# Optimization experiments

Measured on AMD Instinct MI355X. Metric: run time of the kernel, lower is better.

The kernel has to match this reference:

```python
import jax, jax.numpy as jnp
import numpy as np
from jax import lax

B, T, V, E, H = 8, 512, 32000, 256, 512
NEG = -1e9


def setup_inputs() -> dict:
    key = jax.random.key(0)
    ks = jax.random.split(key, 13)
    g = lambda k, shp, sc: (jax.random.normal(k, shp, jnp.float32) * sc)
    return {
        'x': jax.random.randint(ks[0], (B, T), 0, V),
        'lengths': jax.random.randint(ks[1], (B,), T // 2, T + 1),
        'embed': g(ks[2], (V, E), 0.02),
        'W_ih': g(ks[3], (H, E), 1.0 / np.sqrt(E)),
        'W_hh': g(ks[4], (H, H), 1.0 / np.sqrt(H)),
        'b_ih': g(ks[5], (H,), 0.01),
        'b_hh': g(ks[6], (H,), 0.01),
        'attn_W': g(ks[7], (H, 2 * H), 1.0 / np.sqrt(2 * H)),
        'attn_b': g(ks[8], (H,), 0.01),
        'attn_v': g(ks[9], (1, H), 1.0 / np.sqrt(H)),
        'attn_v_b': g(ks[10], (1,), 0.01),
        'fc_W': g(ks[11], (V, 2 * H), 1.0 / np.sqrt(2 * H)),
        'fc_b': g(ks[12], (V,), 0.01),
    }


def reference(x, lengths, embed, W_ih, W_hh, b_ih, b_hh,
              attn_W, attn_b, attn_v, attn_v_b, fc_W, fc_b):
    b, t = x.shape
    h = W_ih.shape[0]
    # embedding with padding_idx=0 (row 0 forced to zero)
    tab = embed.at[0].set(0.0)
    emb = tab[x]  # [B,T,E]
    # vanilla tanh RNN via scan (precompute input projection)
    xin = emb @ W_ih.T + b_ih  # [B,T,H]

    def rnn_step(hprev, xt):
        hnew = jnp.tanh(xt + hprev @ W_hh.T + b_hh)
        return hnew, hnew

    _, out = lax.scan(rnn_step, jnp.zeros((b, h), xin.dtype), xin.transpose(1, 0, 2))
    out = out.transpose(1, 0, 2)  # [B,T,H]
    # pad_packed_sequence zeros hidden states past each sequence length
    len_mask = jnp.arange(t)[None, :] < lengths[:, None]  # [B,T]
    out = out * len_mask[..., None].astype(out.dtype)

    # additive attention: score(t,s) = v . tanh(W1 h_t + W2 h_s + b)
    W1, W2 = attn_W[:, :h], attn_W[:, h:]
    q = out @ W1.T            # [B,T,H]
    k = out @ W2.T + attn_b   # [B,T,H]
    v = attn_v[0]             # [H]

    def att_row(_, qt):  # qt: [B,H] -> scores over all s: [B,T]
        s = jnp.tanh(qt[:, None, :] + k) @ v + attn_v_b[0]
        return None, s

    _, scores = lax.scan(att_row, None, q.transpose(1, 0, 2))  # [T,B,T]
    scores = scores.transpose(1, 0, 2)  # [B,T(query),T(key)]
    causal = jnp.arange(t)[:, None] >= jnp.arange(t)[None, :]  # s <= t
    valid = causal[None] & len_mask[:, None, :]
    scores = jnp.where(valid, scores, NEG)
    alpha = jax.nn.softmax(scores, axis=-1)
    context = jnp.einsum('bts,bsh->bth', alpha, out)  # [B,T,H]
    feats = jnp.concatenate([out, context], axis=-1)  # [B,T,2H]
    logits = feats @ fc_W.T + fc_b  # [B,T,V]
    return logits
```

## Files before the change

kernel.cpp:

```cpp
#include <hip/hip_runtime.h>
#include <hip/hip_bf16.h>

typedef __attribute__((ext_vector_type(8))) short short8;
typedef __attribute__((ext_vector_type(4))) float f32x4;
typedef __attribute__((ext_vector_type(4))) unsigned int u32x4;

__device__ __forceinline__ void glds16(const void* g, void* l) {
  __builtin_amdgcn_global_load_lds(
      (const __attribute__((address_space(1))) unsigned int*)g,
      (__attribute__((address_space(3))) unsigned int*)l, 16, 0, 0);
}

__device__ __forceinline__ void bar_lds() {
  asm volatile("s_waitcnt lgkmcnt(0)\n\ts_barrier" ::: "memory");
}

__device__ __forceinline__ float fast_tanh(float x) {
  float e = __expf(2.0f * x);
  return (e - 1.0f) * __builtin_amdgcn_rcpf(e + 1.0f);
}

__device__ __forceinline__ unsigned short bfh(float f) {
  __hip_bfloat16 h = __float2bfloat16(f);
  return *reinterpret_cast<unsigned short*>(&h);
}
__device__ __forceinline__ float bf2f(unsigned short u) {
  unsigned v = ((unsigned)u) << 16;
  float f;
  __builtin_memcpy(&f, &v, 4);
  return f;
}
__device__ __forceinline__ short bf16r(float f) { return (short)bfh(f); }

union FragU {
  unsigned int u[4];
  short8 s;
};

__global__ __launch_bounds__(256) void k_xin(const int* __restrict__ x, const float* __restrict__ embed,
                                             const float* __restrict__ W_ih, const float* __restrict__ b_ih,
                                             float* __restrict__ xin) {
  __shared__ float At[64][128];
  __shared__ float Bt[128][64];
  const int tid = threadIdx.x;
  const int bt0 = blockIdx.x * 64, j0 = blockIdx.y * 64;
  const int ty = tid >> 4, tx = tid & 15;
  const int lane = tid & 63, cgrp = tid >> 6;
  float acc[4][4] = {};
  for (int kc = 0; kc < 256; kc += 128) {
#pragma unroll
    for (int rr = 0; rr < 8; ++rr) {
      int row = rr * 8 + (tid >> 5);
      int col = (tid & 31) * 4;
      int tok = x[bt0 + row];
      float4 v = make_float4(0.f, 0.f, 0.f, 0.f);
      if (tok != 0) v = *(const float4*)&embed[(size_t)tok * 256 + kc + col];
      *(float4*)&At[row][col] = v;
    }
#pragma unroll
    for (int cc = 0; cc < 8; ++cc) {
      int col = cgrp * 32 + cc * 4;
      float4 v = *(const float4*)&W_ih[(size_t)(j0 + lane) * 256 + kc + col];
      Bt[col + 0][lane] = v.x; Bt[col + 1][lane] = v.y;
      Bt[col + 2][lane] = v.z; Bt[col + 3][lane] = v.w;
    }
    __syncthreads();
    for (int kk = 0; kk < 128; ++kk) {
      float bv[4];
#pragma unroll
      for (int c = 0; c < 4; ++c) bv[c] = Bt[kk][tx * 4 + c];
#pragma unroll
      for (int a = 0; a < 4; ++a) {
        float av = At[ty * 4 + a][kk];
#pragma unroll
        for (int c = 0; c < 4; ++c) acc[a][c] = fmaf(av, bv[c], acc[a][c]);
      }
    }
    __syncthreads();
  }
#pragma unroll
  for (int a = 0; a < 4; ++a) {
    int m = bt0 + ty * 4 + a;
#pragma unroll
    for (int c = 0; c < 4; ++c) {
      int j = j0 + tx * 4 + c;
      xin[(size_t)m * 512 + j] = acc[a][c] + b_ih[j];
    }
  }
}

__global__ __launch_bounds__(512) void k_rnn(const float* __restrict__ xin, const float* __restrict__ W_hh,
                                             const float* __restrict__ b_hh, const int* __restrict__ lengths,
                                             unsigned long long* mbox, float* __restrict__ out,
                                             unsigned short* __restrict__ feats,
                                             const float* __restrict__ fcW, unsigned short* __restrict__ fcWb) {
  const int tid = threadIdx.x;
  if (blockIdx.x >= 8) {
    const size_t stride = (size_t)(gridDim.x - 8) * 512 * 8;
    for (size_t i = ((size_t)(blockIdx.x - 8) * 512 + tid) * 8; i < 32768000ull; i += stride) {
      float4 a = *(const float4*)(fcW + i);
      float4 b = *(const float4*)(fcW + i + 4);
      short8 v;
      v[0] = bf16r(a.x); v[1] = bf16r(a.y); v[2] = bf16r(a.z); v[3] = bf16r(a.w);
      v[4] = bf16r(b.x); v[5] = bf16r(b.y); v[6] = bf16r(b.z); v[7] = bf16r(b.w);
      *(short8*)(fcWb + i) = v;
    }
    return;
  }
  const int blk = blockIdx.x;
  const int w = tid >> 6, l = tid & 63;
  const int jt = w & 3, kh = w >> 2;
  const int j16 = blk * 64 + jt * 16;
  const int r = l & 15;
  const int g = l >> 4;
  const int n = l & 15;

  __shared__ unsigned long long stg[2048];
  __shared__ f32x4 Cbuf[4][64];
  __shared__ float hLf[8][64];
  __shared__ unsigned int hL32[8][64];
  __shared__ int nflag[2];

  short8 bhi[8], blo[8];
  {
    const float* wrow = &W_hh[(size_t)(j16 + n) * 512];
#pragma unroll
    for (int c8 = 0; c8 < 8; ++c8) {
      int c = kh * 8 + c8;
      const float* wp = wrow + c * 32 + g * 8;
      float4 wa = *(const float4*)wp;
      float4 wb = *(const float4*)(wp + 4);
      float wv[8] = {wa.x, wa.y, wa.z, wa.w, wb.x, wb.y, wb.z, wb.w};
#pragma unroll
      for (int e = 0; e < 8; ++e) {
        unsigned short h = bfh(wv[e]);
        bhi[c8][e] = (short)h;
        blo[c8][e] = (short)bfh(wv[e] - bf2f(h));
      }
    }
  }

  float bj = 0.f, xv[4];
  if (w < 4 && l < 32) {
    bj = b_hh[j16 + n];
#pragma unroll
    for (int i = 0; i < 4; ++i)
      xv[i] = xin[((size_t)(g * 4 + i) * 512 + 0) * 512 + j16 + n];
  }
  const int mylen = lengths[(tid >> 6) & 7];

  if (tid < 2) nflag[tid] = 0;
  __syncthreads();

  const int sgran = tid ^ ((tid >> 6) & 3);

  for (int t = 0; t < 512; ++t) {
    {
      unsigned long long* src = mbox + ((size_t)blk * 16 + (t & 15)) * 2048 + tid * 4;
      bool mine = false;
      int round = 0;
      while (true) {
        if (!mine) {
          u32x4 A, B2;
          asm volatile(
              "global_load_dwordx4 %0, %2, off sc0 sc1\n\t"
              "global_load_dwordx4 %1, %2, off offset:16 sc0 sc1\n\t"
              "s_waitcnt vmcnt(0)"
              : "=&v"(A), "=&v"(B2)
              : "v"(src)
              : "memory");
          bool ok = true;
#pragma unroll
          for (int q = 0; q < 4; ++q) ok = ok && (A[q] != 0xFFFFFFFFu) && (B2[q] != 0xFFFFFFFFu);
          if (ok) {
            mine = true;
            stg[sgran * 4 + 0] = (unsigned long long)A[0] | ((unsigned long long)A[1] << 32);
            stg[sgran * 4 + 1] = (unsigned long long)A[2] | ((unsigned long long)A[3] << 32);
            stg[sgran * 4 + 2] = (unsigned long long)B2[0] | ((unsigned long long)B2[1] << 32);
            stg[sgran * 4 + 3] = (unsigned long long)B2[2] | ((unsigned long long)B2[3] << 32);
            u32x4 S;
            S[0] = S[1] = S[2] = S[3] = 0xFFFFFFFFu;
            asm volatile(
                "global_store_dwordx4 %0, %1, off sc0 sc1\n\t"
                "global_store_dwordx4 %0, %1, off offset:16 sc0 sc1"
                :: "v"(src), "v"(S)
                : "memory");
          }
        }
        int p = round & 1;
        if (!mine) nflag[p] = 1;
        bar_lds();
        int bad = nflag[p];
        if (tid == 0) nflag[p ^ 1] = 0;
        bar_lds();
        if (!bad) break;
        if (++round == (1 << 16)) break;
      }
    }

    f32x4 acc0 = {}, acc1 = {};
#pragma unroll
    for (int c8 = 0; c8 < 8; ++c8) {
      FragU ah, al;
      if (r < 8) {
        int gran = r * 64 + kh * 32 + c8 * 4 + g;
        int gs = (gran ^ (r & 3)) * 4;
        unsigned long long u0 = stg[gs + 0], u1 = stg[gs + 1];
        unsigned long long u2 = stg[gs + 2], u3 = stg[gs + 3];
        ah.u[0] = (unsigned)u0; al.u[0] = (unsigned)(u0 >> 32);
        ah.u[1] = (unsigned)u1; al.u[1] = (unsigned)(u1 >> 32);
        ah.u[2] = (unsigned)u2; al.u[2] = (unsigned)(u2 >> 32);
        ah.u[3] = (unsigned)u3; al.u[3] = (unsigned)(u3 >> 32);
      } else {
        ah.u[0] = ah.u[1] = ah.u[2] = ah.u[3] = 0u;
        al.u[0] = al.u[1] = al.u[2] = al.u[3] = 0u;
      }
      if (c8 & 1) {
        acc1 = __builtin_amdgcn_mfma_f32_16x16x32_bf16(ah.s, bhi[c8], acc1, 0, 0, 0);
        acc1 = __builtin_amdgcn_mfma_f32_16x16x32_bf16(ah.s, blo[c8], acc1, 0, 0, 0);
        acc1 = __builtin_amdgcn_mfma_f32_16x16x32_bf16(al.s, bhi[c8], acc1, 0, 0, 0);
      } else {
        acc0 = __builtin_amdgcn_mfma_f32_16x16x32_bf16(ah.s, bhi[c8], acc0, 0, 0, 0);
        acc0 = __builtin_amdgcn_mfma_f32_16x16x32_bf16(ah.s, blo[c8], acc0, 0, 0, 0);
        acc0 = __builtin_amdgcn_mfma_f32_16x16x32_bf16(al.s, bhi[c8], acc0, 0, 0, 0);
      }
    }
    f32x4 tot = acc0 + acc1;

    if (w >= 4) Cbuf[w - 4][l] = tot;
    bar_lds();
    if (w < 4) {
      tot += Cbuf[w][l];
      if (l < 32) {
#pragma unroll
        for (int i = 0; i < 4; ++i) {
          int b = g * 4 + i;
          float hn = fast_tanh(xv[i] + tot[i] + bj);
          hLf[b][jt * 16 + n] = hn;
          unsigned hi = bfh(hn);
          unsigned lo = bfh(hn - bf2f((unsigned short)hi));
          hL32[b][jt * 16 + n] = hi | (lo << 16);
        }
        int tt = (t < 511) ? t + 1 : 511;
#pragma unroll
        for (int i = 0; i < 4; ++i)
          xv[i] = xin[((size_t)(g * 4 + i) * 512 + tt) * 512 + j16 + n];
      }
    }
    bar_lds();

    {
      int b = tid >> 6, jl = tid & 63;
      float hv = hLf[b][jl];
      hv = (t < mylen) ? hv : 0.f;
      out[((size_t)b * 512 + t) * 512 + blk * 64 + jl] = hv;
      feats[((size_t)b * 512 + t) * 1024 + blk * 64 + jl] = bfh(hv);
    }

    if (t < 511) {
      unsigned long long* dst = mbox + ((size_t)w * 16 + ((t + 1) & 15)) * 2048 + blk * 32;
      const int e0 = (l & 15) * 4;
#pragma unroll
      for (int k2 = 0; k2 < 2; ++k2) {
        int b = (l >> 4) + k2 * 4;
        unsigned a0 = hL32[b][e0 + 0], a1 = hL32[b][e0 + 1];
        unsigned a2 = hL32[b][e0 + 2], a3 = hL32[b][e0 + 3];
        u32x4 val;
        val[0] = (a0 & 0xffffu) | (a1 << 16);
        val[1] = (a0 >> 16) | (a1 & 0xffff0000u);
        val[2] = (a2 & 0xffffu) | (a3 << 16);
        val[3] = (a2 >> 16) | (a3 & 0xffff0000u);
        unsigned long long* p = dst + (size_t)b * 256 + (l & 15) * 2;
        asm volatile("global_store_dwordx4 %0, %1, off sc0 sc1" :: "v"(p), "v"(val) : "memory");
      }
    }
  }
}

template <int MODE>
__global__ __launch_bounds__(256) void k_qk(const float* __restrict__ out, const float* __restrict__ attn_W,
                                            const float* __restrict__ attn_b, float* __restrict__ dst) {
  __shared__ float At[64][128];
  __shared__ float Bt[128][64];
  const int tid = threadIdx.x;
  const int bt0 = blockIdx.x * 64, j0 = blockIdx.y * 64;
  const int ty = tid >> 4, tx = tid & 15;
  const int lane = tid & 63, cgrp = tid >> 6;
  float acc[4][4] = {};
  for (int kc = 0; kc < 512; kc += 128) {
#pragma unroll
    for (int rr = 0; rr < 8; ++rr) {
      int row = rr * 8 + (tid >> 5);
      int col = (tid & 31) * 4;
      *(float4*)&At[row][col] = *(const float4*)&out[((size_t)bt0 + row) * 512 + kc + col];
    }
#pragma unroll
    for (int cc = 0; cc < 8; ++cc) {
      int col = cgrp * 32 + cc * 4;
      float4 v = *(const float4*)&attn_W[(size_t)(j0 + lane) * 1024 + (MODE ? 512 : 0) + kc + col];
      Bt[col + 0][lane] = v.x; Bt[col + 1][lane] = v.y;
      Bt[col + 2][lane] = v.z; Bt[col + 3][lane] = v.w;
    }
    __syncthreads();
    for (int kk = 0; kk < 128; ++kk) {
      float bv[4];
#pragma unroll
      for (int c = 0; c < 4; ++c) bv[c] = Bt[kk][tx * 4 + c];
#pragma unroll
      for (int a = 0; a < 4; ++a) {
        float av = At[ty * 4 + a][kk];
#pragma unroll
        for (int c = 0; c < 4; ++c) acc[a][c] = fmaf(av, bv[c], acc[a][c]);
      }
    }
    __syncthreads();
  }
#pragma unroll
  for (int a = 0; a < 4; ++a) {
    int bt = bt0 + ty * 4 + a;
#pragma unroll
    for (int c = 0; c < 4; ++c) {
      int j = j0 + tx * 4 + c;
      if (MODE == 0) {
        dst[(size_t)bt * 512 + j] = acc[a][c];
      } else {
        int bb = bt >> 9, tt = bt & 511;
        dst[((size_t)bb * 512 + j) * 512 + tt] = acc[a][c] + attn_b[j];
      }
    }
  }
}

__global__ __launch_bounds__(256) void k_scores(const float* __restrict__ q, const float* __restrict__ kT,
                                                const float* __restrict__ attn_v, const float* __restrict__ attn_v_b,
                                                const int* __restrict__ lengths, float* __restrict__ pbuf,
                                                float* __restrict__ invl) {
  const int b = blockIdx.x, t0 = blockIdx.y * 4;
  const int tid = threadIdx.x;
  __shared__ float qL[4][512];
  __shared__ float vL[512];
  __shared__ float red[4][4];
  for (int i = tid; i < 4 * 512; i += 256) {
    int rr = i >> 9, h = i & 511;
    qL[rr][h] = q[((size_t)b * 512 + t0 + rr) * 512 + h];
  }
  for (int i = tid; i < 512; i += 256) vL[i] = attn_v[i];
  const float vb = attn_v_b[0];
  const int len = lengths[b];
  __syncthreads();
  const int s_hi = min(t0 + 3, len - 1);
  const float* kTb = kT + (size_t)b * 512 * 512;
  float psum[4] = {0.f, 0.f, 0.f, 0.f};
#pragma unroll
  for (int si = 0; si < 2; ++si) {
    int s = tid + si * 256;
    float acc[4] = {0.f, 0.f, 0.f, 0.f};
    if (s <= s_hi) {
      for (int h = 0; h < 512; ++h) {
        float kv = kTb[(size_t)h * 512 + s];
        float vh = vL[h];
#pragma unroll
        for (int rr = 0; rr < 4; ++rr) acc[rr] = fmaf(vh, fast_tanh(qL[rr][h] + kv), acc[rr]);
      }
    }
#pragma unroll
    for (int rr = 0; rr < 4; ++rr) {
      int t = t0 + rr;
      bool valid = (s <= t) && (s < len);
      float p = valid ? __expf(acc[rr] + vb - 20.f) : 0.f;
      pbuf[((size_t)b * 512 + t) * 512 + s] = p;
      psum[rr] += p;
    }
  }
  const int wv = tid >> 6, ln = tid & 63;
#pragma unroll
  for (int rr = 0; rr < 4; ++rr) {
    float v = psum[rr];
#pragma unroll
    for (int m = 1; m < 64; m <<= 1) v += __shfl_xor(v, m);
    if (ln == 0) red[wv][rr] = v;
  }
  __syncthreads();
  if (tid < 4) {
    float s = red[0][tid] + red[1][tid] + red[2][tid] + red[3][tid];
    invl[(size_t)b * 512 + t0 + tid] = 1.0f / s;
  }
}

__global__ __launch_bounds__(256) void k_context(const float* __restrict__ pbuf, const float* __restrict__ out,
                                                 const float* __restrict__ invl, unsigned short* __restrict__ feats) {
  __shared__ float Pt[64][128];
  __shared__ float Ot[128][64];
  const int b = blockIdx.z, t0 = blockIdx.y * 64, h0 = blockIdx.x * 64;
  const int tid = threadIdx.x, ty = tid >> 4, tx = tid & 15;
  float acc[4][4] = {};
  for (int sc = 0; sc < 512; sc += 128) {
#pragma unroll
    for (int rr = 0; rr < 8; ++rr) {
      int row = rr * 8 + (tid >> 5);
      int col = (tid & 31) * 4;
      *(float4*)&Pt[row][col] = *(const float4*)&pbuf[((size_t)b * 512 + t0 + row) * 512 + sc + col];
    }
#pragma unroll
    for (int rr = 0; rr < 8; ++rr) {
      int srow = rr * 16 + (tid >> 4);
      int col = (tid & 15) * 4;
      *(float4*)&Ot[srow][col] = *(const float4*)&out[((size_t)b * 512 + sc + srow) * 512 + h0 + col];
    }
    __syncthreads();
    for (int kk = 0; kk < 128; ++kk) {
      float ov[4];
#pragma unroll
      for (int c = 0; c < 4; ++c) ov[c] = Ot[kk][tx * 4 + c];
#pragma unroll
      for (int a = 0; a < 4; ++a) {
        float pv = Pt[ty * 4 + a][kk];
#pragma unroll
        for (int c = 0; c < 4; ++c) acc[a][c] = fmaf(pv, ov[c], acc[a][c]);
      }
    }
    __syncthreads();
  }
#pragma unroll
  for (int a = 0; a < 4; ++a) {
    int t = t0 + ty * 4 + a;
    float il = invl[b * 512 + t];
#pragma unroll
    for (int c = 0; c < 4; ++c) {
      int h = h0 + tx * 4 + c;
      feats[((size_t)b * 512 + t) * 1024 + 512 + h] = (unsigned short)bf16r(acc[a][c] * il);
    }
  }
}

__global__ __launch_bounds__(256) void k_logits(const unsigned short* __restrict__ A,
                                                const unsigned short* __restrict__ Bw,
                                                const float* __restrict__ bias, float* __restrict__ C) {
  const int linb = blockIdx.x;
  const int xcd = linb & 7, pos = linb >> 3;
  const int m0 = (xcd * 4 + (pos & 3)) * 128;
  const int n0 = (pos >> 2) * 128;
  __shared__ unsigned short As[128 * 64];
  __shared__ unsigned short Bs[128 * 64];
  const int tid = threadIdx.x;
  const int wave = tid >> 6, lane = tid & 63;
  const int wm = (wave >> 1) * 64, wn = (wave & 1) * 64;
  const int lo16 = lane & 15, oct = lane >> 4;
  f32x4 acc[4][4] = {};
  for (int kt = 0; kt < 1024; kt += 64) {
#pragma unroll
    for (int i = 0; i < 4; ++i) {
      int ci = wave * 4 + i;
      int mrow = ci * 8 + (lane >> 3);
      int k8 = (lane & 7) * 8;
      glds16(&A[(size_t)(m0 + mrow) * 1024 + kt + k8], &As[ci * 512]);
      glds16(&Bw[(size_t)(n0 + mrow) * 1024 + kt + k8], &Bs[ci * 512]);
    }
    __syncthreads();
#pragma unroll
    for (int kk = 0; kk < 2; ++kk) {
      short8 af[4], bf[4];
#pragma unroll
      for (int i = 0; i < 4; ++i)
        af[i] = *(const short8*)&As[(wm + i * 16 + lo16) * 64 + kk * 32 + oct * 8];
#pragma unroll
      for (int jn = 0; jn < 4; ++jn)
        bf[jn] = *(const short8*)&Bs[(wn + jn * 16 + lo16) * 64 + kk * 32 + oct * 8];
#pragma unroll
      for (int i = 0; i < 4; ++i)
#pragma unroll
        for (int jn = 0; jn < 4; ++jn)
          acc[i][jn] = __builtin_amdgcn_mfma_f32_16x16x32_bf16(af[i], bf[jn], acc[i][jn], 0, 0, 0);
    }
    __syncthreads();
  }
#pragma unroll
  for (int jn = 0; jn < 4; ++jn) {
    int nn = n0 + wn + jn * 16 + lo16;
    float bv = bias[nn];
#pragma unroll
    for (int i = 0; i < 4; ++i) {
      int mbase = m0 + wm + i * 16 + oct * 4;
#pragma unroll
      for (int rr = 0; rr < 4; ++rr)
        C[(size_t)(mbase + rr) * 32000 + nn] = acc[i][jn][rr] + bv;
    }
  }
}

extern "C" void kernel_launch(void* const* d_in, const int* in_sizes, int n_in,
                              void* d_out, int out_size, void* d_ws, size_t ws_size,
                              hipStream_t stream) {
  const int* x = (const int*)d_in[0];
  const int* lengths = (const int*)d_in[1];
  const float* embed = (const float*)d_in[2];
  const float* W_ih = (const float*)d_in[3];
  const float* W_hh = (const float*)d_in[4];
  const float* b_ih = (const float*)d_in[5];
  const float* b_hh = (const float*)d_in[6];
  const float* attn_W = (const float*)d_in[7];
  const float* attn_b = (const float*)d_in[8];
  const float* attn_v = (const float*)d_in[9];
  const float* attn_v_b = (const float*)d_in[10];
  const float* fc_W = (const float*)d_in[11];
  const float* fc_b = (const float*)d_in[12];
  float* logits = (float*)d_out;

  char* ws = (char*)d_ws;
  const size_t MB8 = 8388608;
  float* xin  = (float*)(ws);
  float* outp = (float*)(ws + 1 * MB8);
  float* q    = (float*)(ws + 2 * MB8);
  float* kT   = (float*)(ws + 3 * MB8);
  float* pbuf = (float*)(ws + 4 * MB8);
  float* invl = (float*)(ws + 5 * MB8);
  unsigned short* feats = (unsigned short*)(ws + 5 * MB8 + 16384);
  unsigned short* fcWb  = (unsigned short*)(ws + 6 * MB8 + 16384);
  unsigned long long* mbox = (unsigned long long*)pbuf;

  hipMemsetAsync(mbox, 0xFF, 8 * 16 * 16384, stream);
  for (int d = 0; d < 8; ++d)
    hipMemsetAsync((char*)mbox + (size_t)d * 16 * 16384, 0x00, 16384, stream);
  k_xin<<<dim3(64, 8), 256, 0, stream>>>(x, embed, W_ih, b_ih, xin);
  k_rnn<<<136, 512, 0, stream>>>(xin, W_hh, b_hh, lengths, mbox, outp, feats, fc_W, fcWb);
  k_qk<0><<<dim3(64, 8), 256, 0, stream>>>(outp, attn_W, attn_b, q);
  k_qk<1><<<dim3(64, 8), 256, 0, stream>>>(outp, attn_W, attn_b, kT);
  k_scores<<<dim3(8, 128), 256, 0, stream>>>(q, kT, attn_v, attn_v_b, lengths, pbuf, invl);
  k_context<<<dim3(8, 8, 8), 256, 0, stream>>>(pbuf, outp, invl, feats);
  k_logits<<<8000, 256, 0, stream>>>(feats, fcWb, fc_b, logits);
}
```

Before: 2.440 ms.

## Replace block-wide mailbox poll consensus with per-thread spin and merge q/k launches

In the recurrent kernel, each thread now spins on its own mailbox slot until its data arrives, then stages it and issues a single barrier. This replaces the previous loop that ran two LDS barriers per polling round to reach block-wide agreement. It also merges the two q/k projection launches into one grid that uses blockIdx.z to pick the mode, saving one kernel launch and letting both halves run concurrently. The per-thread spin uses a larger guard and relies on each slot being written atomically as one unit.

```diff
diff --git a/kernel.cpp b/kernel.cpp
--- a/kernel.cpp
+++ b/kernel.cpp
@@ -119,7 +119,6 @@
   __shared__ f32x4 Cbuf[4][64];
   __shared__ float hLf[8][64];
   __shared__ unsigned int hL32[8][64];
-  __shared__ int nflag[2];
 
   short8 bhi[8], blo[8];
   {
@@ -149,7 +148,6 @@
   }
   const int mylen = lengths[(tid >> 6) & 7];
 
-  if (tid < 2) nflag[tid] = 0;
   __syncthreads();
 
   const int sgran = tid ^ ((tid >> 6) & 3);
@@ -157,45 +155,33 @@
   for (int t = 0; t < 512; ++t) {
     {
       unsigned long long* src = mbox + ((size_t)blk * 16 + (t & 15)) * 2048 + tid * 4;
-      bool mine = false;
-      int round = 0;
+      u32x4 A, B2;
+      int guard = 0;
       while (true) {
-        if (!mine) {
-          u32x4 A, B2;
-          asm volatile(
-              "global_load_dwordx4 %0, %2, off sc0 sc1\n\t"
-              "global_load_dwordx4 %1, %2, off offset:16 sc0 sc1\n\t"
-              "s_waitcnt vmcnt(0)"
-              : "=&v"(A), "=&v"(B2)
-              : "v"(src)
-              : "memory");
-          bool ok = true;
-#pragma unroll
-          for (int q = 0; q < 4; ++q) ok = ok && (A[q] != 0xFFFFFFFFu) && (B2[q] != 0xFFFFFFFFu);
-          if (ok) {
-            mine = true;
-            stg[sgran * 4 + 0] = (unsigned long long)A[0] | ((unsigned long long)A[1] << 32);
-            stg[sgran * 4 + 1] = (unsigned long long)A[2] | ((unsigned long long)A[3] << 32);
-            stg[sgran * 4 + 2] = (unsigned long long)B2[0] | ((unsigned long long)B2[1] << 32);
-            stg[sgran * 4 + 3] = (unsigned long long)B2[2] | ((unsigned long long)B2[3] << 32);
-            u32x4 S;
-            S[0] = S[1] = S[2] = S[3] = 0xFFFFFFFFu;
-            asm volatile(
-                "global_store_dwordx4 %0, %1, off sc0 sc1\n\t"
-                "global_store_dwordx4 %0, %1, off offset:16 sc0 sc1"
-                :: "v"(src), "v"(S)
-                : "memory");
-          }
-        }
-        int p = round & 1;
-        if (!mine) nflag[p] = 1;
-        bar_lds();
-        int bad = nflag[p];
-        if (tid == 0) nflag[p ^ 1] = 0;
-        bar_lds();
-        if (!bad) break;
-        if (++round == (1 << 16)) break;
-      }
+        asm volatile(
+            "global_load_dwordx4 %0, %2, off sc0 sc1\n\t"
+            "global_load_dwordx4 %1, %2, off offset:16 sc0 sc1\n\t"
+            "s_waitcnt vmcnt(0)"
+            : "=&v"(A), "=&v"(B2)
+            : "v"(src)
+            : "memory");
+        bool ok = true;
+#pragma unroll
+        for (int q = 0; q < 4; ++q) ok = ok && (A[q] != 0xFFFFFFFFu) && (B2[q] != 0xFFFFFFFFu);
+        if (ok || ++guard == (1 << 20)) break;
+      }
+      stg[sgran * 4 + 0] = (unsigned long long)A[0] | ((unsigned long long)A[1] << 32);
+      stg[sgran * 4 + 1] = (unsigned long long)A[2] | ((unsigned long long)A[3] << 32);
+      stg[sgran * 4 + 2] = (unsigned long long)B2[0] | ((unsigned long long)B2[1] << 32);
+      stg[sgran * 4 + 3] = (unsigned long long)B2[2] | ((unsigned long long)B2[3] << 32);
+      u32x4 S;
+      S[0] = S[1] = S[2] = S[3] = 0xFFFFFFFFu;
+      asm volatile(
+          "global_store_dwordx4 %0, %1, off sc0 sc1\n\t"
+          "global_store_dwordx4 %0, %1, off offset:16 sc0 sc1"
+          :: "v"(src), "v"(S)
+          : "memory");
+      bar_lds();
     }
 
     f32x4 acc0 = {}, acc1 = {};
@@ -277,12 +263,13 @@
   }
 }
 
-template <int MODE>
 __global__ __launch_bounds__(256) void k_qk(const float* __restrict__ out, const float* __restrict__ attn_W,
-                                            const float* __restrict__ attn_b, float* __restrict__ dst) {
+                                            const float* __restrict__ attn_b, float* __restrict__ qdst,
+                                            float* __restrict__ kdst) {
   __shared__ float At[64][128];
   __shared__ float Bt[128][64];
   const int tid = threadIdx.x;
+  const int MODE = blockIdx.z;
   const int bt0 = blockIdx.x * 64, j0 = blockIdx.y * 64;
   const int ty = tid >> 4, tx = tid & 15;
   const int lane = tid & 63, cgrp = tid >> 6;
@@ -322,10 +309,10 @@
     for (int c = 0; c < 4; ++c) {
       int j = j0 + tx * 4 + c;
       if (MODE == 0) {
-        dst[(size_t)bt * 512 + j] = acc[a][c];
+        qdst[(size_t)bt * 512 + j] = acc[a][c];
       } else {
         int bb = bt >> 9, tt = bt & 511;
-        dst[((size_t)bb * 512 + j) * 512 + tt] = acc[a][c] + attn_b[j];
+        kdst[((size_t)bb * 512 + j) * 512 + tt] = acc[a][c] + attn_b[j];
       }
     }
   }
@@ -523,8 +510,7 @@
     hipMemsetAsync((char*)mbox + (size_t)d * 16 * 16384, 0x00, 16384, stream);
   k_xin<<<dim3(64, 8), 256, 0, stream>>>(x, embed, W_ih, b_ih, xin);
   k_rnn<<<136, 512, 0, stream>>>(xin, W_hh, b_hh, lengths, mbox, outp, feats, fc_W, fcWb);
-  k_qk<0><<<dim3(64, 8), 256, 0, stream>>>(outp, attn_W, attn_b, q);
-  k_qk<1><<<dim3(64, 8), 256, 0, stream>>>(outp, attn_W, attn_b, kT);
+  k_qk<<<dim3(64, 8, 2), 256, 0, stream>>>(outp, attn_W, attn_b, q, kT);
   k_scores<<<dim3(8, 128), 256, 0, stream>>>(q, kT, attn_v, attn_v_b, lengths, pbuf, invl);
   k_context<<<dim3(8, 8, 8), 256, 0, stream>>>(pbuf, outp, invl, feats);
   k_logits<<<8000, 256, 0, stream>>>(feats, fcWb, fc_b, logits);
```

Result: faster. 2.250 ms (-7.8%).
